# Kernel optimization log

Hardware: AMD Instinct MI355X
Metric: run time of the kernel (lower is better)

The kernel has to match this reference:

```python
import jax, jax.numpy as jnp
import numpy as np
from jax import lax

HID = 128      # GNN hidden dim (node_label_embedding_size)
EMB = 64       # char-CNN output (graph_node_label_representation_size)
N_LAYERS = 6
N_ETYPES = 12
CHAR_EMB = 16
KW = 5         # conv kernel width
LEAKY = 0.2


def _gru(x, h, k, rk, b):
    # keras-style GRU cell: gates z, r, candidate hh; new h = z*h + (1-z)*hh
    H = h.shape[-1]
    g = x @ k + b                       # [N, 3H]
    z = jax.nn.sigmoid(g[:, :H] + h @ rk[:, :H])
    r = jax.nn.sigmoid(g[:, H:2 * H] + h @ rk[:, H:2 * H])
    hh = jnp.tanh(g[:, 2 * H:] + (r * h) @ rk[:, 2 * H:])
    return z * h + (1.0 - z) * hh


def setup_inputs() -> dict:
    key = jax.random.key(0)
    ks = jax.random.split(key, 32)
    N, U, L, E, G = 100000, 20000, 16, 100000, 64
    inp = {}
    inp["graphs_in_batch"] = G
    inp["node_labels_unique"] = jax.random.randint(ks[0], (U, L), 0, 256, dtype=jnp.int32)
    inp["node_labels_index"] = jax.random.randint(ks[1], (N,), 0, U, dtype=jnp.int32)
    inp["node_to_graph"] = jnp.sort(jax.random.randint(ks[2], (N,), 0, G, dtype=jnp.int32))
    inp["regression_labels"] = jax.random.normal(ks[3], (G,), dtype=jnp.float32)
    for t in range(N_ETYPES):
        inp[f"adj_{t}"] = jax.random.randint(ks[4 + t], (E, 2), 0, N, dtype=jnp.int32)
    # learned params
    inp["char_embed"] = jax.random.normal(ks[16], (256, CHAR_EMB), dtype=jnp.float32) * 0.1
    inp["conv_w"] = jax.random.normal(ks[17], (KW, CHAR_EMB, EMB), dtype=jnp.float32) / np.sqrt(KW * CHAR_EMB)
    inp["conv_b"] = jnp.zeros((EMB,), dtype=jnp.float32)
    inp["W_msg"] = jax.random.normal(ks[18], (N_LAYERS, N_ETYPES, HID, HID), dtype=jnp.float32) / np.sqrt(HID)
    inp["gru_k"] = jax.random.normal(ks[19], (N_LAYERS, HID, 3 * HID), dtype=jnp.float32) / np.sqrt(HID)
    inp["gru_rk"] = jax.random.normal(ks[20], (N_LAYERS, HID, 3 * HID), dtype=jnp.float32) / np.sqrt(HID)
    inp["gru_b"] = jnp.zeros((N_LAYERS, 3 * HID), dtype=jnp.float32)
    inp["score_w"] = jax.random.normal(ks[21], (HID, 1), dtype=jnp.float32) / np.sqrt(HID)
    inp["score_b"] = jnp.zeros((1,), dtype=jnp.float32)
    inp["mlp_w1"] = jax.random.normal(ks[22], (HID, 128), dtype=jnp.float32) / np.sqrt(HID)
    inp["mlp_b1"] = jnp.zeros((128,), dtype=jnp.float32)
    inp["mlp_w2"] = jax.random.normal(ks[23], (128, 32), dtype=jnp.float32) / np.sqrt(128)
    inp["mlp_b2"] = jnp.zeros((32,), dtype=jnp.float32)
    inp["mlp_w3"] = jax.random.normal(ks[24], (32, 8), dtype=jnp.float32) / np.sqrt(32)
    inp["mlp_b3"] = jnp.zeros((8,), dtype=jnp.float32)
    inp["mlp_w4"] = jax.random.normal(ks[25], (8, 1), dtype=jnp.float32) / np.sqrt(8)
    inp["mlp_b4"] = jnp.zeros((1,), dtype=jnp.float32)
    return inp


def reference(graphs_in_batch, node_labels_unique, node_labels_index, node_to_graph,
              regression_labels, adj_0, adj_1, adj_2, adj_3, adj_4, adj_5, adj_6,
              adj_7, adj_8, adj_9, adj_10, adj_11, char_embed, conv_w, conv_b,
              W_msg, gru_k, gru_rk, gru_b, score_w, score_b,
              mlp_w1, mlp_b1, mlp_w2, mlp_b2, mlp_w3, mlp_b3, mlp_w4, mlp_b4):
    adj = jnp.stack([adj_0, adj_1, adj_2, adj_3, adj_4, adj_5, adj_6,
                     adj_7, adj_8, adj_9, adj_10, adj_11])  # [T, E, 2]
    # --- char-CNN node label embedding ---
    chars = char_embed[node_labels_unique]                  # [U, L, CE]
    conv = lax.conv_general_dilated(chars, conv_w, (1,), 'SAME',
                                    dimension_numbers=('NWC', 'WIO', 'NWC'))
    label_rep = jnp.max(jax.nn.relu(conv + conv_b), axis=1)  # [U, EMB]
    feats = label_rep[node_labels_index]                     # [N, EMB]
    N = feats.shape[0]
    # pad initial features up to hidden_dim
    h = jnp.pad(feats, ((0, 0), (0, HID - EMB)))             # [N, HID]
    src = adj[:, :, 0]                                       # [T, E]
    tgt = adj[:, :, 1].reshape(-1)                           # [T*E]
    # --- 6-layer GGNN message passing ---
    for layer in range(N_LAYERS):
        h_src = h[src]                                       # [T, E, HID]
        msgs = jnp.einsum('teh,thd->ted', h_src, W_msg[layer])
        agg = jax.ops.segment_sum(msgs.reshape(-1, HID), tgt, num_segments=N)
        h = _gru(agg, h, gru_k[layer], gru_rk[layer], gru_b[layer])
    # --- weighted-sum graph readout (sigmoid weights, leaky_relu MLP) ---
    scores = jax.nn.sigmoid(h @ score_w + score_b)           # [N, 1]
    v = jax.nn.leaky_relu(h @ mlp_w1 + mlp_b1, LEAKY)
    v = jax.nn.leaky_relu(v @ mlp_w2 + mlp_b2, LEAKY)
    v = jax.nn.leaky_relu(v @ mlp_w3 + mlp_b3, LEAKY)
    v = v @ mlp_w4 + mlp_b4                                  # [N, 1]
    graph_rep = jax.ops.segment_sum(scores * v, node_to_graph,
                                    num_segments=graphs_in_batch)  # [G, 1]
    return graph_rep
```

## Files before the change

kernel.cpp:

```cpp
#include <hip/hip_runtime.h>
#include <hip/hip_bf16.h>

#define LEAKY_SLOPE 0.2f

typedef short short8 __attribute__((ext_vector_type(8)));
typedef short short4v __attribute__((ext_vector_type(4)));
typedef float f32x4 __attribute__((ext_vector_type(4)));

static inline int cdiv(int a, int b) { return (a + b - 1) / b; }

__device__ __forceinline__ float bf2f(unsigned short s) {
    return __uint_as_float(((unsigned int)s) << 16);
}
__device__ __forceinline__ unsigned short f2bf(float x) {
    unsigned int u = __float_as_uint(x);
    return (unsigned short)((u + 0x7FFFu + ((u >> 16) & 1u)) >> 16);
}
__device__ __forceinline__ unsigned short bf_hi(float x, float& rem) {
    unsigned int u = __float_as_uint(x);
    unsigned int hi = (u + 0x7FFFu + ((u >> 16) & 1u)) & 0xFFFF0000u;
    rem = x - __uint_as_float(hi);
    return (unsigned short)(hi >> 16);
}

struct EdgeArgs {
    const int* adj[12];
    int E[12];
    int colOff[12];
};

__global__ __launch_bounds__(64) void label_kernel(
    const int* __restrict__ labels, const float* __restrict__ char_embed,
    const float* __restrict__ conv_w, const float* __restrict__ conv_b,
    float* __restrict__ lr, int U)
{
    __shared__ float ch[20][16];
    __shared__ int lab[16];
    const int u = blockIdx.x, t = threadIdx.x;
    {
        const int r = t >> 4, i = t & 15;
        const int padrow[4] = {0, 1, 18, 19};
        ch[padrow[r]][i] = 0.f;
    }
    if (t < 16) lab[t] = labels[(size_t)u * 16 + t];
    float cwr[5][16];
    #pragma unroll
    for (int k = 0; k < 5; ++k)
        #pragma unroll
        for (int i = 0; i < 16; ++i)
            cwr[k][i] = conv_w[(k * 16 + i) * 64 + t];
    __syncthreads();
    for (int j = t; j < 256; j += 64)
        ch[2 + (j >> 4)][j & 15] = char_embed[(size_t)lab[j >> 4] * 16 + (j & 15)];
    __syncthreads();
    float aw[16];
    const float b = conv_b[t];
    #pragma unroll
    for (int w = 0; w < 16; ++w) aw[w] = b;
    #pragma unroll
    for (int x = 0; x < 20; ++x)
        #pragma unroll
        for (int i = 0; i < 16; ++i) {
            const float chv = ch[x][i];
            #pragma unroll
            for (int k = 0; k < 5; ++k) {
                const int w = x - k;
                if (w >= 0 && w < 16) aw[w] += chv * cwr[k][i];
            }
        }
    float m = 0.f;
    #pragma unroll
    for (int w = 0; w < 16; ++w) m = fmaxf(m, aw[w]);
    lr[(size_t)u * 64 + t] = m;
}

__global__ void init_h_split(const int* __restrict__ idx, const float* __restrict__ lr,
                             unsigned short* __restrict__ hS, int N, int NP)
{
    const int i = blockIdx.x * blockDim.x + threadIdx.x;
    if (i >= NP * 16) return;
    const int n = i >> 4, kg = i & 15;
    const size_t u = (size_t)(n >> 7) * 32768 + (size_t)kg * 1024 + (size_t)(n & 127) * 8;
    short8 hi, lo;
    if (n < N && kg < 8) {
        const int id = idx[n];
        #pragma unroll
        for (int j = 0; j < 8; ++j) {
            const float v = lr[(size_t)id * 64 + kg * 8 + j];
            float r; hi[j] = (short)bf_hi(v, r); lo[j] = (short)f2bf(r);
        }
    } else {
        #pragma unroll
        for (int j = 0; j < 8; ++j) { hi[j] = 0; lo[j] = 0; }
    }
    *(short8*)(hS + u) = hi;
    *(short8*)(hS + u + 16384) = lo;
}

__global__ void hist_kernel(EdgeArgs ea, int* __restrict__ deg, int N)
{
    const int t = blockIdx.y;
    const int e = blockIdx.x * blockDim.x + threadIdx.x;
    if (e >= ea.E[t]) return;
    atomicAdd(&deg[(size_t)t * N + ea.adj[t][2 * e + 1]], 1);
}

__global__ __launch_bounds__(256) void scan_a(const int* __restrict__ deg,
                                              int* __restrict__ partial, int N, int nchunk)
{
    const int t = blockIdx.y, b = blockIdx.x;
    const int base = b * 2048;
    int s = 0;
    for (int i = threadIdx.x; i < 2048; i += 256) {
        const int g = base + i;
        if (g < N) s += deg[(size_t)t * N + g];
    }
    __shared__ int sm[256];
    sm[threadIdx.x] = s; __syncthreads();
    for (int off = 128; off > 0; off >>= 1) {
        if (threadIdx.x < off) sm[threadIdx.x] += sm[threadIdx.x + off];
        __syncthreads();
    }
    if (threadIdx.x == 0) partial[t * nchunk + b] = sm[0];
}

__global__ void scan_b(int* __restrict__ partial, int nchunk)
{
    const int t = threadIdx.x;
    if (t >= 12) return;
// ... 41 lines not shown
                            int* __restrict__ cursor, int* __restrict__ col, int N)
{
    const int t = blockIdx.y;
    const int e = blockIdx.x * blockDim.x + threadIdx.x;
    if (e >= ea.E[t]) return;
    const int s  = ea.adj[t][2 * e];
    const int tg = ea.adj[t][2 * e + 1];
    const int pos = rowptr[(size_t)t * (N + 1) + tg] + atomicAdd(&cursor[(size_t)t * N + tg], 1);
    col[ea.colOff[t] + pos] = s;
}

struct WSrc { const float* wmsg; const float* gk; const float* grk; const float* w1; };

__global__ void split_w_kernel(WSrc s, unsigned short* __restrict__ wb, int nmat)
{
    const int gidx = blockIdx.x * 256 + threadIdx.x;
    const int m = gidx >> 14, e = gidx & 16383;
    if (m >= nmat) return;
    const int kg = e >> 10, rem = e & 1023, c = rem >> 3, j = rem & 7;
    const int k = kg * 8 + j;
    float x;
    if (m < 72) x = s.wmsg[(size_t)m * 16384 + (size_t)k * 128 + c];
    else if (m < 108) {
        const int g = m - 72, layer = g / 6, r2 = g % 6;
        const float* base = (r2 < 3) ? s.gk : s.grk;
        const int slice = r2 % 3;
        x = base[(size_t)layer * 49152 + (size_t)k * 384 + slice * 128 + c];
    } else x = s.w1[(size_t)k * 128 + c];
    float r; const unsigned short hi = bf_hi(x, r);
    wb[(size_t)m * 32768 + e] = hi;
    wb[(size_t)m * 32768 + 16384 + e] = f2bf(r);
}

__device__ __forceinline__ void stage_panel(const unsigned short* __restrict__ g,
                                            unsigned short* __restrict__ lds, int tid)
{
    #pragma unroll
    for (int i = 0; i < 16; ++i) {
        const int uo = i * 2048 + tid * 8;
        *(short8*)(lds + uo) = *(const short8*)(g + uo);
    }
}

template<int NM>
__device__ __forceinline__ void mfma_pass(const unsigned short* __restrict__ lds,
                                          const unsigned short* const* Bs,
                                          f32x4 (&acc)[NM][4][4],
                                          int wr, int wc, int lrow, int lkg)
{
    #pragma unroll 1
    for (int c = 0; c < 4; ++c) {
        const int kg = c * 4 + lkg;
        short8 ah[4], al[4];
        #pragma unroll
        for (int m = 0; m < 4; ++m) {
            const int u = kg * 1024 + (wr * 64 + m * 16 + lrow) * 8;
            ah[m] = *(const short8*)(lds + u);
            al[m] = *(const short8*)(lds + u + 16384);
        }
        #pragma unroll
        for (int t = 0; t < NM; ++t) {
            const unsigned short* __restrict__ B = Bs[t];
            short8 bh[4], bl[4];
            #pragma unroll
            for (int n = 0; n < 4; ++n) {
                const int u = kg * 1024 + (wc * 64 + n * 16 + lrow) * 8;
                bh[n] = *(const short8*)(B + u);
                bl[n] = *(const short8*)(B + u + 16384);
            }
            #pragma unroll
            for (int m = 0; m < 4; ++m)
                #pragma unroll
                for (int n = 0; n < 4; ++n) {
                    acc[t][m][n] = __builtin_amdgcn_mfma_f32_16x16x32_bf16(ah[m], bh[n], acc[t][m][n], 0, 0, 0);
                    acc[t][m][n] = __builtin_amdgcn_mfma_f32_16x16x32_bf16(ah[m], bl[n], acc[t][m][n], 0, 0, 0);
                    acc[t][m][n] = __builtin_amdgcn_mfma_f32_16x16x32_bf16(al[m], bh[n], acc[t][m][n], 0, 0, 0);
                }
        }
    }
}

template<int NM>
__global__ __launch_bounds__(256) void msg_kernel(
    const unsigned short* __restrict__ hS,
    const unsigned short* __restrict__ B0, const unsigned short* __restrict__ B1,
    float* __restrict__ out0, float* __restrict__ out1)
{
    __shared__ unsigned short lds[32768];
    const int tid = threadIdx.x;
    stage_panel(hS + (size_t)blockIdx.x * 32768, lds, tid);
    const int wave = tid >> 6, lane = tid & 63;
    const int wr = wave >> 1, wc = wave & 1, lrow = lane & 15, lkg = lane >> 4;
    f32x4 acc[NM][4][4] = {};
    __syncthreads();
    const unsigned short* Bs[2] = {B0, B1};
    mfma_pass<NM>(lds, Bs, acc, wr, wc, lrow, lkg);
    const size_t rowBase = (size_t)blockIdx.x * 128;
    #pragma unroll
    for (int t = 0; t < NM; ++t) {
        float* __restrict__ op = t ? out1 : out0;
        #pragma unroll
        for (int m = 0; m < 4; ++m)
            #pragma unroll
            for (int n = 0; n < 4; ++n) {
                const int col = wc * 64 + n * 16 + lrow;
                #pragma unroll
                for (int i = 0; i < 4; ++i) {
                    const size_t r = rowBase + wr * 64 + m * 16 + lkg * 4 + i;
                    op[r * 128 + col] = acc[t][m][n][i];
                }
            }
    }
}

__global__ __launch_bounds__(256) void zr_kernel(
    const unsigned short* __restrict__ aT, const unsigned short* __restrict__ hS,
    const unsigned short* __restrict__ k0, const unsigned short* __restrict__ k1,
    const unsigned short* __restrict__ rk0, const unsigned short* __restrict__ rk1,
    const float* __restrict__ bias,
    float* __restrict__ zOut, unsigned short* __restrict__ rhS)
{
    __shared__ unsigned short lds[32768];
    const int tid = threadIdx.x;
    const size_t pbase = (size_t)blockIdx.x * 32768;
    const int wave = tid >> 6, lane = tid & 63;
    const int wr = wave >> 1, wc = wave & 1, lrow = lane & 15, lkg = lane >> 4;
    f32x4 acc[2][4][4] = {};

    stage_panel(aT + pbase, lds, tid);
    __syncthreads();
    { const unsigned short* Bs[2] = {k0, k1};  mfma_pass<2>(lds, Bs, acc, wr, wc, lrow, lkg); }
    __syncthreads();
    stage_panel(hS + pbase, lds, tid);
    __syncthreads();
    { const unsigned short* Bs[2] = {rk0, rk1}; mfma_pass<2>(lds, Bs, acc, wr, wc, lrow, lkg); }

    const size_t rowBase = (size_t)blockIdx.x * 128;
    #pragma unroll
    for (int m = 0; m < 4; ++m)
        #pragma unroll
        for (int n = 0; n < 4; ++n) {
            const int col = wc * 64 + n * 16 + lrow;
            #pragma unroll
            for (int i = 0; i < 4; ++i) {
                const int rl = wr * 64 + m * 16 + lkg * 4 + i;
                const float z = 1.f / (1.f + __expf(-(acc[0][m][n][i] + bias[col])));
                zOut[(rowBase + rl) * 128 + col] = z;
                const float v = 1.f / (1.f + __expf(-(acc[1][m][n][i] + bias[128 + col])));
                const int hu = (col >> 3) * 1024 + rl * 8 + (col & 7);
                const float hval = bf2f(lds[hu]) + bf2f(lds[hu + 16384]);
                const float rh = v * hval;
                float rem; const unsigned short hi = bf_hi(rh, rem);
                rhS[pbase + hu] = hi;
                rhS[pbase + hu + 16384] = f2bf(rem);
            }
        }
}

__global__ __launch_bounds__(256) void gemm_lds(
    const unsigned short* __restrict__ A1, const unsigned short* __restrict__ B1,
    const unsigned short* __restrict__ A2, const unsigned short* __restrict__ B2,
    const float* __restrict__ bias, float* __restrict__ outF, int act)
{
    __shared__ unsigned short lds[32768];
    const int tid = threadIdx.x;
    const size_t pbase = (size_t)blockIdx.x * 32768;
    const int wave = tid >> 6, lane = tid & 63;
    const int wr = wave >> 1, wc = wave & 1, lrow = lane & 15, lkg = lane >> 4;
    f32x4 acc[1][4][4] = {};

    stage_panel(A1 + pbase, lds, tid);
    __syncthreads();
    { const unsigned short* Bs[2] = {B1, nullptr}; mfma_pass<1>(lds, Bs, acc, wr, wc, lrow, lkg); }
    if (A2) {
        __syncthreads();
        stage_panel(A2 + pbase, lds, tid);
        __syncthreads();
        const unsigned short* Bs[2] = {B2, nullptr};
        mfma_pass<1>(lds, Bs, acc, wr, wc, lrow, lkg);
    }
    const size_t rowBase = (size_t)blockIdx.x * 128;
    #pragma unroll
    for (int m = 0; m < 4; ++m)
        #pragma unroll
        for (int n = 0; n < 4; ++n) {
            const int col = wc * 64 + n * 16 + lrow;
            #pragma unroll
            for (int i = 0; i < 4; ++i) {
                const int rl = wr * 64 + m * 16 + lkg * 4 + i;
                float v = acc[0][m][n][i];
                if (bias) v += bias[col];
                if (act == 1) v = v > 0.f ? v : LEAKY_SLOPE * v;
                outF[(rowBase + rl) * 128 + col] = v;
            }
        }
}

__global__ __launch_bounds__(256) void gather_csr(
    const int* __restrict__ rowptr, const int* __restrict__ col,
    const float* __restrict__ M, float* __restrict__ agg, int N, int accum)
{
    const int i = blockIdx.x * blockDim.x + threadIdx.x;
    const int n = i >> 5, q = i & 31;
    if (n >= N) return;
    float4 acc;
    if (accum) acc = *reinterpret_cast<const float4*>(agg + (size_t)n * 128 + (q << 2));
    else       acc = make_float4(0.f, 0.f, 0.f, 0.f);
    for (int s = rowptr[n]; s < rowptr[n + 1]; ++s) {
        const float4 v = *reinterpret_cast<const float4*>(M + (size_t)col[s] * 128 + (q << 2));
        acc.x += v.x; acc.y += v.y; acc.z += v.z; acc.w += v.w;
    }
    *reinterpret_cast<float4*>(agg + (size_t)n * 128 + (q << 2)) = acc;
}

__global__ __launch_bounds__(256) void gather2_csr(
    const int* __restrict__ rp0, const int* __restrict__ c0, const float* __restrict__ M0,
    const int* __restrict__ rp1, const int* __restrict__ c1, const float* __restrict__ M1,
    float* __restrict__ agg, int N, int accum)
{
    const int i = blockIdx.x * blockDim.x + threadIdx.x;
    const int n = i >> 5, q = i & 31;
    if (n >= N) return;
    float4 acc;
    if (accum) acc = *reinterpret_cast<const float4*>(agg + (size_t)n * 128 + (q << 2));
    else       acc = make_float4(0.f, 0.f, 0.f, 0.f);
    for (int s = rp0[n]; s < rp0[n + 1]; ++s) {
        const float4 v = *reinterpret_cast<const float4*>(M0 + (size_t)c0[s] * 128 + (q << 2));
        acc.x += v.x; acc.y += v.y; acc.z += v.z; acc.w += v.w;
    }
    for (int s = rp1[n]; s < rp1[n + 1]; ++s) {
        const float4 v = *reinterpret_cast<const float4*>(M1 + (size_t)c1[s] * 128 + (q << 2));
        acc.x += v.x; acc.y += v.y; acc.z += v.z; acc.w += v.w;
    }
    *reinterpret_cast<float4*>(agg + (size_t)n * 128 + (q << 2)) = acc;
}

__global__ __launch_bounds__(256) void gather_split_csr(
    const int* __restrict__ rp, const int* __restrict__ cl, const float* __restrict__ M,
    const float* __restrict__ agg, unsigned short* __restrict__ aT, int N, int NP)
{
    const int i = blockIdx.x * blockDim.x + threadIdx.x;
    const int n = i >> 5, q = i & 31;
    if (n >= NP) return;
    float4 a = make_float4(0.f, 0.f, 0.f, 0.f);
    if (n < N) {
        a = *reinterpret_cast<const float4*>(agg + (size_t)n * 128 + (q << 2));
        for (int s = rp[n]; s < rp[n + 1]; ++s) {
            const float4 v = *reinterpret_cast<const float4*>(M + (size_t)cl[s] * 128 + (q << 2));
            a.x += v.x; a.y += v.y; a.z += v.z; a.w += v.w;
        }
    }
    const size_t u = (size_t)(n >> 7) * 32768 + (size_t)(q >> 1) * 1024
                   + (size_t)(n & 127) * 8 + (q & 1) * 4;
    const float vv[4] = {a.x, a.y, a.z, a.w};
    short4v hi, lo;
    #pragma unroll
    for (int j = 0; j < 4; ++j) {
        float r; hi[j] = (short)bf_hi(vv[j], r); lo[j] = (short)f2bf(r);
    }
    *(short4v*)(aT + u) = hi;
    *(short4v*)(aT + u + 16384) = lo;
}

__global__ void gru_ew2_split(const float* __restrict__ Z, const float* __restrict__ G,
                              unsigned short* __restrict__ hS, int N)
{
    const int i = blockIdx.x * blockDim.x + threadIdx.x;
    if (i >= N * 16) return;
    const int n = i >> 4, kg = i & 15;
    const size_t u = (size_t)(n >> 7) * 32768 + (size_t)kg * 1024 + (size_t)(n & 127) * 8;
    const short8 hi = *(const short8*)(hS + u);
    const short8 lo = *(const short8*)(hS + u + 16384);
    const size_t ro = (size_t)n * 128 + kg * 8;
    short8 nhi, nlo;
    #pragma unroll
    for (int j = 0; j < 8; ++j) {
        const float h = bf2f((unsigned short)hi[j]) + bf2f((unsigned short)lo[j]);
        const float z = Z[ro + j];
        const float hn = z * h + (1.f - z) * tanhf(G[ro + j]);
        float r; nhi[j] = (short)bf_hi(hn, r); nlo[j] = (short)f2bf(r);
    }
    *(short8*)(hS + u) = nhi;
    *(short8*)(hS + u + 16384) = nlo;
}

__global__ __launch_bounds__(256) void final_kernel(
    const unsigned short* __restrict__ hS, const float* __restrict__ V1,
    const int* __restrict__ n2g,
    const float* __restrict__ w2, const float* __restrict__ b2,
    const float* __restrict__ w3, const float* __restrict__ b3,
    const float* __restrict__ w4, const float* __restrict__ b4,
    const float* __restrict__ score_w, const float* __restrict__ score_b,
    float* __restrict__ out, int N)
{
    const int n = blockIdx.x * blockDim.x + threadIdx.x;
    const int nc = n < N ? n : N - 1;
    const int g = n2g[nc];

    float sp = score_b[0];
    #pragma unroll 4
    for (int kg = 0; kg < 16; ++kg) {
        const size_t u = (size_t)(nc >> 7) * 32768 + (size_t)kg * 1024 + (size_t)(nc & 127) * 8;
        const short8 hh = *(const short8*)(hS + u);
        const short8 hl = *(const short8*)(hS + u + 16384);
        #pragma unroll
        for (int j = 0; j < 8; ++j)
            sp += (bf2f((unsigned short)hh[j]) + bf2f((unsigned short)hl[j])) * score_w[kg * 8 + j];
    }

    float V2[32];
    #pragma unroll
    for (int j = 0; j < 32; ++j) V2[j] = b2[j];
    #pragma unroll 2
    for (int k = 0; k < 128; k += 4) {
        const float4 v1 = *reinterpret_cast<const float4*>(V1 + (size_t)nc * 128 + k);
        const float vv[4] = {v1.x, v1.y, v1.z, v1.w};
        #pragma unroll
        for (int kk = 0; kk < 4; ++kk)
            #pragma unroll
            for (int j = 0; j < 32; ++j)
                V2[j] += vv[kk] * w2[(k + kk) * 32 + j];
    }
    #pragma unroll
    for (int j = 0; j < 32; ++j) { const float x = V2[j]; V2[j] = x > 0.f ? x : LEAKY_SLOPE * x; }

    float V3[8];
    #pragma unroll
    for (int j = 0; j < 8; ++j) V3[j] = b3[j];
    #pragma unroll
    for (int k = 0; k < 32; ++k)
        #pragma unroll
        for (int j = 0; j < 8; ++j) V3[j] += V2[k] * w3[k * 8 + j];
    #pragma unroll
    for (int j = 0; j < 8; ++j) { const float x = V3[j]; V3[j] = x > 0.f ? x : LEAKY_SLOPE * x; }

    float o4 = b4[0];
    #pragma unroll
// ... 30 lines not shown
        if (ea.E[t] > Emax) Emax = ea.E[t];
    }
    const float* char_embed = (const float*)d_in[17];
    const float* conv_w     = (const float*)d_in[18];
    const float* conv_b     = (const float*)d_in[19];
    const float* W_msg      = (const float*)d_in[20];
    const float* gru_k      = (const float*)d_in[21];
    const float* gru_rk     = (const float*)d_in[22];
    const float* gru_b      = (const float*)d_in[23];
    const float* score_w    = (const float*)d_in[24];
    const float* score_b    = (const float*)d_in[25];
    const float* w1 = (const float*)d_in[26];
    const float* b1 = (const float*)d_in[27];
    const float* w2 = (const float*)d_in[28];
    const float* b2 = (const float*)d_in[29];
    const float* w3 = (const float*)d_in[30];
    const float* b3 = (const float*)d_in[31];
    const float* w4 = (const float*)d_in[32];
    const float* b4 = (const float*)d_in[33];

    const int N = in_sizes[2];
    const int U = in_sizes[1] / 16;
    const int G = out_size;
    float* out = (float*)d_out;

    const int NPB = cdiv(N, 128);
    const int NP  = NPB * 128;
    const int NCHUNK = cdiv(N, 2048);
    const int NMAT = 109;

    float* ws = (float*)d_ws;
    size_t o = 0;
    float* lr   = ws + o; o += (size_t)U * 64;
    float* hSf  = ws + o; o += (size_t)NP * 128;
    float* Mf   = ws + o; o += (size_t)NP * 128;
    float* aggf = ws + o; o += (size_t)NP * 128;
    float* rhf  = ws + o; o += (size_t)NP * 128;
    float* wbf  = ws + o; o += (size_t)NMAT * 16384;
    int* rowptr = (int*)(ws + o);
    int* colarr = rowptr + (size_t)12 * (N + 1);
    const size_t total_bytes = o * sizeof(float)
        + ((size_t)12 * (N + 1) + (size_t)Etot) * sizeof(int);
    if (total_bytes > ws_size) return;

    unsigned short* hS  = (unsigned short*)hSf;
    unsigned short* aT  = (unsigned short*)Mf;
    unsigned short* rhS = (unsigned short*)rhf;
    unsigned short* wb  = (unsigned short*)wbf;

    int* deg     = (int*)Mf;
    int* cursor  = deg + (size_t)12 * N;
    int* partial = cursor + (size_t)12 * N;

    hipMemsetAsync(d_out, 0, (size_t)G * sizeof(float), stream);
    hipMemsetAsync(deg, 0, ((size_t)24 * N + 12 * NCHUNK) * sizeof(int), stream);

    {
        const dim3 ge(cdiv(Emax, 256), 12);
        const dim3 gs(NCHUNK, 12);
        hist_kernel<<<ge, 256, 0, stream>>>(ea, deg, N);
        scan_a<<<gs, 256, 0, stream>>>(deg, partial, N, NCHUNK);
        scan_b<<<1, 64, 0, stream>>>(partial, NCHUNK);
        scan_c<<<gs, 256, 0, stream>>>(deg, partial, rowptr, N, NCHUNK);
        fill_kernel<<<ge, 256, 0, stream>>>(ea, rowptr, cursor, colarr, N);
    }

    WSrc wsrc{W_msg, gru_k, gru_rk, w1};
    split_w_kernel<<<cdiv(NMAT * 16384, 256), 256, 0, stream>>>(wsrc, wb, NMAT);
    label_kernel<<<U, 64, 0, stream>>>(labels, char_embed, conv_w, conv_b, lr, U);
    init_h_split<<<cdiv(NP * 16, 256), 256, 0, stream>>>(nidx, lr, hS, N, NP);

    const int gatherBlocks = cdiv(N * 32, 256);
    const int gatherBlocksNP = cdiv(NP * 32, 256);
    const int ewBlocks = cdiv(N * 16, 256);
    auto rp  = [&](int t) { return rowptr + (size_t)t * (N + 1); };
    auto cp  = [&](int t) { return colarr + ea.colOff[t]; };
    auto wbm = [&](int m) { return wb + (size_t)m * 32768; };

    for (int layer = 0; layer < 6; ++layer) {
        const float* bl = gru_b + (size_t)layer * 384;
        const int mk = 72 + layer * 6;
        for (int p = 0; p < 5; ++p) {
            const int t0 = 2 * p, t1 = 2 * p + 1;
            msg_kernel<2><<<NPB, 256, 0, stream>>>(hS, wbm(layer * 12 + t0), wbm(layer * 12 + t1), Mf, rhf);
            gather2_csr<<<gatherBlocks, 256, 0, stream>>>(rp(t0), cp(t0), Mf,
                                                          rp(t1), cp(t1), rhf, aggf, N, p > 0);
        }
        msg_kernel<1><<<NPB, 256, 0, stream>>>(hS, wbm(layer * 12 + 10), nullptr, Mf, nullptr);
        gather_csr<<<gatherBlocks, 256, 0, stream>>>(rp(10), cp(10), Mf, aggf, N, 1);
        msg_kernel<1><<<NPB, 256, 0, stream>>>(hS, wbm(layer * 12 + 11), nullptr, rhf, nullptr);
        gather_split_csr<<<gatherBlocksNP, 256, 0, stream>>>(rp(11), cp(11), rhf, aggf, aT, N, NP);
        zr_kernel<<<NPB, 256, 0, stream>>>(aT, hS, wbm(mk + 0), wbm(mk + 1),
                                           wbm(mk + 3), wbm(mk + 4), bl, aggf, rhS);
        gemm_lds<<<NPB, 256, 0, stream>>>(aT, wbm(mk + 2), rhS, wbm(mk + 5), bl + 256, Mf, 0);
        gru_ew2_split<<<ewBlocks, 256, 0, stream>>>(aggf, Mf, hS, N);
    }
    gemm_lds<<<NPB, 256, 0, stream>>>(hS, wbm(108), nullptr, nullptr, b1, Mf, 1);
    final_kernel<<<cdiv(N, 256), 256, 0, stream>>>(hS, Mf, n2g, w2, b2, w3, b3, w4, b4,
                                                   score_w, score_b, out, N);
}
```

Baseline: 4.307 ms.

## Aggregate neighbor features before message GEMM and fuse GRU stages with pipelined LDS

Reorders message passing from transform-then-scatter to gather-then-transform: each block sums source node features per edge type via CSR, then runs one K=12*128 GEMM against the stacked per-type weights. This removes the per-type full-N message GEMMs and the fp32 message buffers that the gather kernels had to read back. Node state moves to a row-interleaved hi/lo bf16 layout, and the GRU is folded into two double-buffered GEMM kernels with swizzled LDS that also apply the elementwise update. The gather now runs inside the GEMM kernel with irregular per-row degree loops, so load imbalance and gather latency may stall the MFMA pipeline.

Result: slower. 4.518 ms (+4.9%).

```diff
diff --git a/kernel.cpp b/kernel.cpp
--- a/kernel.cpp
+++ b/kernel.cpp
@@ -4,7 +4,6 @@
 #define LEAKY_SLOPE 0.2f
 
 typedef short short8 __attribute__((ext_vector_type(8)));
-typedef short short4v __attribute__((ext_vector_type(4)));
 typedef float f32x4 __attribute__((ext_vector_type(4)));
 
 static inline int cdiv(int a, int b) { return (a + b - 1) / b; }
@@ -28,6 +27,7 @@
     int E[12];
     int colOff[12];
 };
+struct ColPtrs { const int* c[12]; };
 
 __global__ __launch_bounds__(64) void label_kernel(
     const int* __restrict__ labels, const float* __restrict__ char_embed,
@@ -74,14 +74,15 @@
     lr[(size_t)u * 64 + t] = m;
 }
 
-__global__ void init_h_split(const int* __restrict__ idx, const float* __restrict__ lr,
-                             unsigned short* __restrict__ hS, int N, int NP)
+__global__ void init_hP(const int* __restrict__ idx, const float* __restrict__ lr,
+                        unsigned short* __restrict__ hP, int N, int NP)
 {
     const int i = blockIdx.x * blockDim.x + threadIdx.x;
     if (i >= NP * 16) return;
     const int n = i >> 4, kg = i & 15;
-    const size_t u = (size_t)(n >> 7) * 32768 + (size_t)kg * 1024 + (size_t)(n & 127) * 8;
     short8 hi, lo;
+    #pragma unroll
+    for (int j = 0; j < 8; ++j) { hi[j] = 0; lo[j] = 0; }
     if (n < N && kg < 8) {
         const int id = idx[n];
         #pragma unroll
@@ -89,12 +90,9 @@
             const float v = lr[(size_t)id * 64 + kg * 8 + j];
             float r; hi[j] = (short)bf_hi(v, r); lo[j] = (short)f2bf(r);
         }
-    } else {
-        #pragma unroll
-        for (int j = 0; j < 8; ++j) { hi[j] = 0; lo[j] = 0; }
-    }
-    *(short8*)(hS + u) = hi;
-    *(short8*)(hS + u + 16384) = lo;
+    }
+    *(short8*)(hP + (size_t)n * 256 + kg * 16) = hi;
+    *(short8*)(hP + (size_t)n * 256 + kg * 16 + 8) = lo;
 }
 
 __global__ void hist_kernel(EdgeArgs ea, int* __restrict__ deg, int N)
@@ -202,110 +200,202 @@
     wb[(size_t)m * 32768 + 16384 + e] = f2bf(r);
 }
 
-__device__ __forceinline__ void stage_panel(const unsigned short* __restrict__ g,
-                                            unsigned short* __restrict__ lds, int tid)
-{
-    #pragma unroll
-    for (int i = 0; i < 16; ++i) {
-        const int uo = i * 2048 + tid * 8;
-        *(short8*)(lds + uo) = *(const short8*)(g + uo);
-    }
-}
-
-template<int NM>
-__device__ __forceinline__ void mfma_pass(const unsigned short* __restrict__ lds,
-                                          const unsigned short* const* Bs,
-                                          f32x4 (&acc)[NM][4][4],
-                                          int wr, int wc, int lrow, int lkg)
-{
-    #pragma unroll 1
-    for (int c = 0; c < 4; ++c) {
-        const int kg = c * 4 + lkg;
-        short8 ah[4], al[4];
-        #pragma unroll
-        for (int m = 0; m < 4; ++m) {
-            const int u = kg * 1024 + (wr * 64 + m * 16 + lrow) * 8;
-            ah[m] = *(const short8*)(lds + u);
-            al[m] = *(const short8*)(lds + u + 16384);
-        }
-        #pragma unroll
-        for (int t = 0; t < NM; ++t) {
-            const unsigned short* __restrict__ B = Bs[t];
-            short8 bh[4], bl[4];
-            #pragma unroll
-            for (int n = 0; n < 4; ++n) {
-                const int u = kg * 1024 + (wc * 64 + n * 16 + lrow) * 8;
-                bh[n] = *(const short8*)(B + u);
-                bl[n] = *(const short8*)(B + u + 16384);
-            }
-            #pragma unroll
-            for (int m = 0; m < 4; ++m)
-                #pragma unroll
-                for (int n = 0; n < 4; ++n) {
-                    acc[t][m][n] = __builtin_amdgcn_mfma_f32_16x16x32_bf16(ah[m], bh[n], acc[t][m][n], 0, 0, 0);
-                    acc[t][m][n] = __builtin_amdgcn_mfma_f32_16x16x32_bf16(ah[m], bl[n], acc[t][m][n], 0, 0, 0);
-                    acc[t][m][n] = __builtin_amdgcn_mfma_f32_16x16x32_bf16(al[m], bh[n], acc[t][m][n], 0, 0, 0);
-                }
-        }
-    }
-}
-
-template<int NM>
-__global__ __launch_bounds__(256) void msg_kernel(
-    const unsigned short* __restrict__ hS,
-    const unsigned short* __restrict__ B0, const unsigned short* __restrict__ B1,
-    float* __restrict__ out0, float* __restrict__ out1)
-{
-    __shared__ unsigned short lds[32768];
-    const int tid = threadIdx.x;
-    stage_panel(hS + (size_t)blockIdx.x * 32768, lds, tid);
+__global__ __launch_bounds__(256) void agg_kernel(
+    const unsigned short* __restrict__ hP,
+    const int* __restrict__ rowptr,
+    ColPtrs cps,
+    const unsigned short* __restrict__ wbL,
+    float* __restrict__ agg, int N)
+{
+    __shared__ unsigned short lds[2][8192];
+    const int tid = threadIdx.x, p = blockIdx.x;
+    const int r_loc = tid >> 1;
+    const int R = p * 128 + r_loc;
+    const int kp = (tid & 1) * 2;
     const int wave = tid >> 6, lane = tid & 63;
     const int wr = wave >> 1, wc = wave & 1, lrow = lane & 15, lkg = lane >> 4;
-    f32x4 acc[NM][4][4] = {};
+    f32x4 acc[4][4] = {};
+    float ga[2][8];
+
+    auto gather = [&](int s) {
+        const int t = s >> 2, q = s & 3;
+        #pragma unroll
+        for (int pc = 0; pc < 2; ++pc)
+            #pragma unroll
+            for (int j = 0; j < 8; ++j) ga[pc][j] = 0.f;
+        if (R < N) {
+            const int rbase = t * (N + 1) + R;
+            const int e1 = rowptr[rbase + 1];
+            const int* __restrict__ cl = cps.c[t];
+            for (int e = rowptr[rbase]; e < e1; ++e) {
+                const size_t sb = (size_t)cl[e] * 256 + (size_t)(q * 4 + kp) * 16;
+                #pragma unroll
+                for (int pc = 0; pc < 2; ++pc) {
+                    const short8 hh = *(const short8*)(hP + sb + pc * 16);
+                    const short8 hl = *(const short8*)(hP + sb + pc * 16 + 8);
+                    #pragma unroll
+                    for (int j = 0; j < 8; ++j)
+                        ga[pc][j] += bf2f((unsigned short)hh[j]) + bf2f((unsigned short)hl[j]);
+                }
+            }
+        }
+    };
+    auto stq = [&](int buf) {
+        unsigned short* L = lds[buf];
+        #pragma unroll
+        for (int pc = 0; pc < 2; ++pc) {
+            short8 hi, lo;
+            #pragma unroll
+            for (int j = 0; j < 8; ++j) {
+                float rem; hi[j] = (short)bf_hi(ga[pc][j], rem); lo[j] = (short)f2bf(rem);
+            }
+            const int kgl = kp + pc;
+            const int u = (kgl * 1024 + r_loc * 8) ^ (kgl << 3);
+            *(short8*)(L + u) = hi;
+            *(short8*)(L + u + 4096) = lo;
+        }
+    };
+    auto mfma_q = [&](int buf, int s) {
+        const unsigned short* L = lds[buf];
+        const unsigned short* __restrict__ B = wbL + (size_t)(s >> 2) * 32768;
+        const int q = s & 3;
+        short8 ah[4], al[4];
+        #pragma unroll
+        for (int m = 0; m < 4; ++m) {
+            const int u = ((lkg << 10) + (wr * 64 + m * 16 + lrow) * 8) ^ (lkg << 3);
+            ah[m] = *(const short8*)(L + u);
+            al[m] = *(const short8*)(L + u + 4096);
+        }
+        #pragma unroll
+        for (int n = 0; n < 4; ++n) {
+            const int ub = (q * 4 + lkg) * 1024 + (wc * 64 + n * 16 + lrow) * 8;
+            const short8 bh = *(const short8*)(B + ub);
+            const short8 bl = *(const short8*)(B + ub + 16384);
+            #pragma unroll
+            for (int m = 0; m < 4; ++m) {
+                acc[m][n] = __builtin_amdgcn_mfma_f32_16x16x32_bf16(ah[m], bh, acc[m][n], 0, 0, 0);
+                acc[m][n] = __builtin_amdgcn_mfma_f32_16x16x32_bf16(ah[m], bl, acc[m][n], 0, 0, 0);
+                acc[m][n] = __builtin_amdgcn_mfma_f32_16x16x32_bf16(al[m], bh, acc[m][n], 0, 0, 0);
+            }
+        }
+    };
+
+    gather(0); stq(0); gather(1);
     __syncthreads();
-    const unsigned short* Bs[2] = {B0, B1};
-    mfma_pass<NM>(lds, Bs, acc, wr, wc, lrow, lkg);
-    const size_t rowBase = (size_t)blockIdx.x * 128;
-    #pragma unroll
-    for (int t = 0; t < NM; ++t) {
-        float* __restrict__ op = t ? out1 : out0;
-        #pragma unroll
-        for (int m = 0; m < 4; ++m)
-            #pragma unroll
-            for (int n = 0; n < 4; ++n) {
-                const int col = wc * 64 + n * 16 + lrow;
-                #pragma unroll
-                for (int i = 0; i < 4; ++i) {
-                    const size_t r = rowBase + wr * 64 + m * 16 + lkg * 4 + i;
-                    op[r * 128 + col] = acc[t][m][n][i];
-                }
-            }
-    }
-}
-
-__global__ __launch_bounds__(256) void zr_kernel(
-    const unsigned short* __restrict__ aT, const unsigned short* __restrict__ hS,
+    #pragma unroll 1
+    for (int s = 0; s < 48; ++s) {
+        mfma_q(s & 1, s);
+        if (s < 47) {
+            stq((s + 1) & 1);
+            if (s < 46) gather(s + 2);
+            __syncthreads();
+        }
+    }
+
+    #pragma unroll
+    for (int m = 0; m < 4; ++m)
+        #pragma unroll
+        for (int n = 0; n < 4; ++n) {
+            const int col = wc * 64 + n * 16 + lrow;
+            #pragma unroll
+            for (int i = 0; i < 4; ++i) {
+                const size_t Rg = (size_t)p * 128 + wr * 64 + m * 16 + lkg * 4 + i;
+                agg[Rg * 128 + col] = acc[m][n][i];
+            }
+        }
+}
+
+__global__ __launch_bounds__(256) void zr2_kernel(
+    const float* __restrict__ aggf, const unsigned short* __restrict__ hP,
     const unsigned short* __restrict__ k0, const unsigned short* __restrict__ k1,
     const unsigned short* __restrict__ rk0, const unsigned short* __restrict__ rk1,
     const float* __restrict__ bias,
-    float* __restrict__ zOut, unsigned short* __restrict__ rhS)
-{
-    __shared__ unsigned short lds[32768];
-    const int tid = threadIdx.x;
-    const size_t pbase = (size_t)blockIdx.x * 32768;
+    float* __restrict__ Zf, unsigned short* __restrict__ rhP)
+{
+    __shared__ unsigned short lds[2][8192];
+    const int tid = threadIdx.x, p = blockIdx.x;
     const int wave = tid >> 6, lane = tid & 63;
     const int wr = wave >> 1, wc = wave & 1, lrow = lane & 15, lkg = lane >> 4;
     f32x4 acc[2][4][4] = {};
-
-    stage_panel(aT + pbase, lds, tid);
+    float fv[16];
+    short8 ph[2], pl[2];
+
+    auto ldq = [&](int s) {
+        const int q = s & 3;
+        #pragma unroll
+        for (int j = 0; j < 2; ++j) {
+            const int cid = j * 256 + tid, kgl = cid >> 7, row = cid & 127;
+            if (s < 4) {
+                const float* a = aggf + ((size_t)p * 128 + row) * 128 + q * 32 + kgl * 8;
+                const float4 v0 = *(const float4*)(a);
+                const float4 v1 = *(const float4*)(a + 4);
+                fv[j*8+0]=v0.x; fv[j*8+1]=v0.y; fv[j*8+2]=v0.z; fv[j*8+3]=v0.w;
+                fv[j*8+4]=v1.x; fv[j*8+5]=v1.y; fv[j*8+6]=v1.z; fv[j*8+7]=v1.w;
+            } else {
+                const unsigned short* hp = hP + ((size_t)p * 128 + row) * 256 + (q * 4 + kgl) * 16;
+                ph[j] = *(const short8*)(hp);
+                pl[j] = *(const short8*)(hp + 8);
+            }
+        }
+    };
+    auto stq = [&](int buf, int s) {
+        unsigned short* L = lds[buf];
+        #pragma unroll
+        for (int j = 0; j < 2; ++j) {
+            const int cid = j * 256 + tid, kgl = cid >> 7, row = cid & 127;
+            const int u = (kgl * 1024 + row * 8) ^ (kgl << 3);
+            short8 hi, lo;
+            if (s < 4) {
+                #pragma unroll
+                for (int q8 = 0; q8 < 8; ++q8) {
+                    float rem; hi[q8] = (short)bf_hi(fv[j*8+q8], rem); lo[q8] = (short)f2bf(rem);
+                }
+            } else { hi = ph[j]; lo = pl[j]; }
+            *(short8*)(L + u) = hi;
+            *(short8*)(L + u + 4096) = lo;
+        }
+    };
+    auto mfma_q = [&](int buf, int s) {
+        const unsigned short* L = lds[buf];
+        const int q = s & 3;
+        short8 ah[4], al[4];
+        #pragma unroll
+        for (int m = 0; m < 4; ++m) {
+            const int u = ((lkg << 10) + (wr * 64 + m * 16 + lrow) * 8) ^ (lkg << 3);
+            ah[m] = *(const short8*)(L + u);
+            al[m] = *(const short8*)(L + u + 4096);
+        }
+        const unsigned short* Bt[2] = { (s < 4) ? k0 : rk0, (s < 4) ? k1 : rk1 };
+        #pragma unroll
+        for (int t = 0; t < 2; ++t) {
+            const unsigned short* __restrict__ B = Bt[t];
+            #pragma unroll
+            for (int n = 0; n < 4; ++n) {
+                const int ub = (q * 4 + lkg) * 1024 + (wc * 64 + n * 16 + lrow) * 8;
+                const short8 bh = *(const short8*)(B + ub);
+                const short8 bl = *(const short8*)(B + ub + 16384);
+                #pragma unroll
+                for (int m = 0; m < 4; ++m) {
+                    acc[t][m][n] = __builtin_amdgcn_mfma_f32_16x16x32_bf16(ah[m], bh, acc[t][m][n], 0, 0, 0);
+                    acc[t][m][n] = __builtin_amdgcn_mfma_f32_16x16x32_bf16(ah[m], bl, acc[t][m][n], 0, 0, 0);
+                    acc[t][m][n] = __builtin_amdgcn_mfma_f32_16x16x32_bf16(al[m], bh, acc[t][m][n], 0, 0, 0);
+                }
+            }
+        }
+    };
+
+    ldq(0); stq(0, 0); ldq(1);
     __syncthreads();
-    { const unsigned short* Bs[2] = {k0, k1};  mfma_pass<2>(lds, Bs, acc, wr, wc, lrow, lkg); }
-    __syncthreads();
-    stage_panel(hS + pbase, lds, tid);
-    __syncthreads();
-    { const unsigned short* Bs[2] = {rk0, rk1}; mfma_pass<2>(lds, Bs, acc, wr, wc, lrow, lkg); }
-
-    const size_t rowBase = (size_t)blockIdx.x * 128;
+    #pragma unroll
+    for (int s = 0; s < 8; ++s) {
+        mfma_q(s & 1, s);
+        if (s < 7) {
+            stq((s + 1) & 1, s + 1);
+            if (s < 6) ldq(s + 2);
+            __syncthreads();
+        }
+    }
+
     #pragma unroll
     for (int m = 0; m < 4; ++m)
         #pragma unroll
@@ -314,42 +404,105 @@
             #pragma unroll
             for (int i = 0; i < 4; ++i) {
                 const int rl = wr * 64 + m * 16 + lkg * 4 + i;
+                const size_t R = (size_t)p * 128 + rl;
                 const float z = 1.f / (1.f + __expf(-(acc[0][m][n][i] + bias[col])));
-                zOut[(rowBase + rl) * 128 + col] = z;
-                const float v = 1.f / (1.f + __expf(-(acc[1][m][n][i] + bias[128 + col])));
-                const int hu = (col >> 3) * 1024 + rl * 8 + (col & 7);
-                const float hval = bf2f(lds[hu]) + bf2f(lds[hu + 16384]);
-                const float rh = v * hval;
-                float rem; const unsigned short hi = bf_hi(rh, rem);
-                rhS[pbase + hu] = hi;
-                rhS[pbase + hu + 16384] = f2bf(rem);
-            }
-        }
-}
-
-__global__ __launch_bounds__(256) void gemm_lds(
-    const unsigned short* __restrict__ A1, const unsigned short* __restrict__ B1,
-    const unsigned short* __restrict__ A2, const unsigned short* __restrict__ B2,
-    const float* __restrict__ bias, float* __restrict__ outF, int act)
-{
-    __shared__ unsigned short lds[32768];
-    const int tid = threadIdx.x;
-    const size_t pbase = (size_t)blockIdx.x * 32768;
+                Zf[R * 128 + col] = z;
+                const float r = 1.f / (1.f + __expf(-(acc[1][m][n][i] + bias[128 + col])));
+                const size_t hu = R * 256 + (size_t)(col >> 3) * 16 + (col & 7);
+                const float h = bf2f(hP[hu]) + bf2f(hP[hu + 8]);
+                float rem; const unsigned short hh = bf_hi(r * h, rem);
+                rhP[hu] = hh;
+                rhP[hu + 8] = f2bf(rem);
+            }
+        }
+}
+
+__global__ __launch_bounds__(256) void g2_kernel(
+    const float* __restrict__ aggf, const unsigned short* __restrict__ rhP,
+    const unsigned short* __restrict__ k2, const unsigned short* __restrict__ rk2,
+    const float* __restrict__ bias, const float* __restrict__ Zf,
+    unsigned short* __restrict__ hP)
+{
+    __shared__ unsigned short lds[2][8192];
+    const int tid = threadIdx.x, p = blockIdx.x;
     const int wave = tid >> 6, lane = tid & 63;
     const int wr = wave >> 1, wc = wave & 1, lrow = lane & 15, lkg = lane >> 4;
-    f32x4 acc[1][4][4] = {};
-
-    stage_panel(A1 + pbase, lds, tid);
+    f32x4 acc[4][4] = {};
+    float fv[16];
+    short8 ph[2], pl[2];
+
+    auto ldq = [&](int s) {
+        const int q = s & 3;
+        #pragma unroll
+        for (int j = 0; j < 2; ++j) {
+            const int cid = j * 256 + tid, kgl = cid >> 7, row = cid & 127;
+            if (s < 4) {
+                const float* a = aggf + ((size_t)p * 128 + row) * 128 + q * 32 + kgl * 8;
+                const float4 v0 = *(const float4*)(a);
+                const float4 v1 = *(const float4*)(a + 4);
+                fv[j*8+0]=v0.x; fv[j*8+1]=v0.y; fv[j*8+2]=v0.z; fv[j*8+3]=v0.w;
+                fv[j*8+4]=v1.x; fv[j*8+5]=v1.y; fv[j*8+6]=v1.z; fv[j*8+7]=v1.w;
+            } else {
+                const unsigned short* hp = rhP + ((size_t)p * 128 + row) * 256 + (q * 4 + kgl) * 16;
+                ph[j] = *(const short8*)(hp);
+                pl[j] = *(const short8*)(hp + 8);
+            }
+        }
+    };
+    auto stq = [&](int buf, int s) {
+        unsigned short* L = lds[buf];
+        #pragma unroll
+        for (int j = 0; j < 2; ++j) {
+            const int cid = j * 256 + tid, kgl = cid >> 7, row = cid & 127;
+            const int u = (kgl * 1024 + row * 8) ^ (kgl << 3);
+            short8 hi, lo;
+            if (s < 4) {
+                #pragma unroll
+                for (int q8 = 0; q8 < 8; ++q8) {
+                    float rem; hi[q8] = (short)bf_hi(fv[j*8+q8], rem); lo[q8] = (short)f2bf(rem);
+                }
+            } else { hi = ph[j]; lo = pl[j]; }
+            *(short8*)(L + u) = hi;
+            *(short8*)(L + u + 4096) = lo;
+        }
+    };
+    auto mfma_q = [&](int buf, int s) {
+        const unsigned short* L = lds[buf];
+        const int q = s & 3;
+        short8 ah[4], al[4];
+        #pragma unroll
+        for (int m = 0; m < 4; ++m) {
+            const int u = ((lkg << 10) + (wr * 64 + m * 16 + lrow) * 8) ^ (lkg << 3);
+            ah[m] = *(const short8*)(L + u);
+            al[m] = *(const short8*)(L + u + 4096);
+        }
+        const unsigned short* __restrict__ B = (s < 4) ? k2 : rk2;
+        #pragma unroll
+        for (int n = 0; n < 4; ++n) {
+            const int ub = (q * 4 + lkg) * 1024 + (wc * 64 + n * 16 + lrow) * 8;
+            const short8 bh = *(const short8*)(B + ub);
+            const short8 bl = *(const short8*)(B + ub + 16384);
+            #pragma unroll
+            for (int m = 0; m < 4; ++m) {
+                acc[m][n] = __builtin_amdgcn_mfma_f32_16x16x32_bf16(ah[m], bh, acc[m][n], 0, 0, 0);
+                acc[m][n] = __builtin_amdgcn_mfma_f32_16x16x32_bf16(ah[m], bl, acc[m][n], 0, 0, 0);
+                acc[m][n] = __builtin_amdgcn_mfma_f32_16x16x32_bf16(al[m], bh, acc[m][n], 0, 0, 0);
+            }
+        }
+    };
+
+    ldq(0); stq(0, 0); ldq(1);
     __syncthreads();
-    { const unsigned short* Bs[2] = {B1, nullptr}; mfma_pass<1>(lds, Bs, acc, wr, wc, lrow, lkg); }
-    if (A2) {
-        __syncthreads();
-        stage_panel(A2 + pbase, lds, tid);
-        __syncthreads();
-        const unsigned short* Bs[2] = {B2, nullptr};
-        mfma_pass<1>(lds, Bs, acc, wr, wc, lrow, lkg);
-    }
-    const size_t rowBase = (size_t)blockIdx.x * 128;
+    #pragma unroll
+    for (int s = 0; s < 8; ++s) {
+        mfma_q(s & 1, s);
+        if (s < 7) {
+            stq((s + 1) & 1, s + 1);
+            if (s < 6) ldq(s + 2);
+            __syncthreads();
+        }
+    }
+
     #pragma unroll
     for (int m = 0; m < 4; ++m)
         #pragma unroll
@@ -358,104 +511,101 @@
             #pragma unroll
             for (int i = 0; i < 4; ++i) {
                 const int rl = wr * 64 + m * 16 + lkg * 4 + i;
-                float v = acc[0][m][n][i];
-                if (bias) v += bias[col];
-                if (act == 1) v = v > 0.f ? v : LEAKY_SLOPE * v;
-                outF[(rowBase + rl) * 128 + col] = v;
-            }
-        }
-}
-
-__global__ __launch_bounds__(256) void gather_csr(
-    const int* __restrict__ rowptr, const int* __restrict__ col,
-    const float* __restrict__ M, float* __restrict__ agg, int N, int accum)
-{
-    const int i = blockIdx.x * blockDim.x + threadIdx.x;
-    const int n = i >> 5, q = i & 31;
-    if (n >= N) return;
-    float4 acc;
-    if (accum) acc = *reinterpret_cast<const float4*>(agg + (size_t)n * 128 + (q << 2));
-    else       acc = make_float4(0.f, 0.f, 0.f, 0.f);
-    for (int s = rowptr[n]; s < rowptr[n + 1]; ++s) {
-        const float4 v = *reinterpret_cast<const float4*>(M + (size_t)col[s] * 128 + (q << 2));
-        acc.x += v.x; acc.y += v.y; acc.z += v.z; acc.w += v.w;
-    }
-    *reinterpret_cast<float4*>(agg + (size_t)n * 128 + (q << 2)) = acc;
-}
-
-__global__ __launch_bounds__(256) void gather2_csr(
-    const int* __restrict__ rp0, const int* __restrict__ c0, const float* __restrict__ M0,
-    const int* __restrict__ rp1, const int* __restrict__ c1, const float* __restrict__ M1,
-    float* __restrict__ agg, int N, int accum)
-{
-    const int i = blockIdx.x * blockDim.x + threadIdx.x;
-    const int n = i >> 5, q = i & 31;
-    if (n >= N) return;
-    float4 acc;
-    if (accum) acc = *reinterpret_cast<const float4*>(agg + (size_t)n * 128 + (q << 2));
-    else       acc = make_float4(0.f, 0.f, 0.f, 0.f);
-    for (int s = rp0[n]; s < rp0[n + 1]; ++s) {
-        const float4 v = *reinterpret_cast<const float4*>(M0 + (size_t)c0[s] * 128 + (q << 2));
-        acc.x += v.x; acc.y += v.y; acc.z += v.z; acc.w += v.w;
-    }
-    for (int s = rp1[n]; s < rp1[n + 1]; ++s) {
-        const float4 v = *reinterpret_cast<const float4*>(M1 + (size_t)c1[s] * 128 + (q << 2));
-        acc.x += v.x; acc.y += v.y; acc.z += v.z; acc.w += v.w;
-    }
-    *reinterpret_cast<float4*>(agg + (size_t)n * 128 + (q << 2)) = acc;
-}
-
-__global__ __launch_bounds__(256) void gather_split_csr(
-    const int* __restrict__ rp, const int* __restrict__ cl, const float* __restrict__ M,
-    const float* __restrict__ agg, unsigned short* __restrict__ aT, int N, int NP)
-{
-    const int i = blockIdx.x * blockDim.x + threadIdx.x;
-    const int n = i >> 5, q = i & 31;
-    if (n >= NP) return;
-    float4 a = make_float4(0.f, 0.f, 0.f, 0.f);
-    if (n < N) {
-        a = *reinterpret_cast<const float4*>(agg + (size_t)n * 128 + (q << 2));
-        for (int s = rp[n]; s < rp[n + 1]; ++s) {
-            const float4 v = *reinterpret_cast<const float4*>(M + (size_t)cl[s] * 128 + (q << 2));
-            a.x += v.x; a.y += v.y; a.z += v.z; a.w += v.w;
-        }
-    }
-    const size_t u = (size_t)(n >> 7) * 32768 + (size_t)(q >> 1) * 1024
-                   + (size_t)(n & 127) * 8 + (q & 1) * 4;
-    const float vv[4] = {a.x, a.y, a.z, a.w};
-    short4v hi, lo;
-    #pragma unroll
-    for (int j = 0; j < 4; ++j) {
-        float r; hi[j] = (short)bf_hi(vv[j], r); lo[j] = (short)f2bf(r);
-    }
-    *(short4v*)(aT + u) = hi;
-    *(short4v*)(aT + u + 16384) = lo;
-}
-
-__global__ void gru_ew2_split(const float* __restrict__ Z, const float* __restrict__ G,
-                              unsigned short* __restrict__ hS, int N)
-{
-    const int i = blockIdx.x * blockDim.x + threadIdx.x;
-    if (i >= N * 16) return;
-    const int n = i >> 4, kg = i & 15;
-    const size_t u = (size_t)(n >> 7) * 32768 + (size_t)kg * 1024 + (size_t)(n & 127) * 8;
-    const short8 hi = *(const short8*)(hS + u);
-    const short8 lo = *(const short8*)(hS + u + 16384);
-    const size_t ro = (size_t)n * 128 + kg * 8;
-    short8 nhi, nlo;
-    #pragma unroll
-    for (int j = 0; j < 8; ++j) {
-        const float h = bf2f((unsigned short)hi[j]) + bf2f((unsigned short)lo[j]);
-        const float z = Z[ro + j];
-        const float hn = z * h + (1.f - z) * tanhf(G[ro + j]);
-        float r; nhi[j] = (short)bf_hi(hn, r); nlo[j] = (short)f2bf(r);
-    }
-    *(short8*)(hS + u) = nhi;
-    *(short8*)(hS + u + 16384) = nlo;
+                const size_t R = (size_t)p * 128 + rl;
+                const float g = acc[m][n][i] + bias[col];
+                const size_t hu = R * 256 + (size_t)(col >> 3) * 16 + (col & 7);
+                const float h = bf2f(hP[hu]) + bf2f(hP[hu + 8]);
+                const float z = Zf[R * 128 + col];
+                const float hn = z * h + (1.f - z) * tanhf(g);
+                float rem; const unsigned short hh = bf_hi(hn, rem);
+                hP[hu] = hh;
+                hP[hu + 8] = f2bf(rem);
+            }
+        }
+}
+
+__global__ __launch_bounds__(256) void v1_kernel(
+    const unsigned short* __restrict__ hP, const unsigned short* __restrict__ w1b,
+    const float* __restrict__ bias, float* __restrict__ outF)
+{
+    __shared__ unsigned short lds[2][8192];
+    const int tid = threadIdx.x, p = blockIdx.x;
+    const int wave = tid >> 6, lane = tid & 63;
+    const int wr = wave >> 1, wc = wave & 1, lrow = lane & 15, lkg = lane >> 4;
+    f32x4 acc[4][4] = {};
+    short8 ph[2], pl[2];
+
+    auto ldq = [&](int s) {
+        #pragma unroll
+        for (int j = 0; j < 2; ++j) {
+            const int cid = j * 256 + tid, kgl = cid >> 7, row = cid & 127;
+            const unsigned short* hp = hP + ((size_t)p * 128 + row) * 256 + (s * 4 + kgl) * 16;
+            ph[j] = *(const short8*)(hp);
+            pl[j] = *(const short8*)(hp + 8);
+        }
+    };
+    auto stq = [&](int buf) {
+        unsigned short* L = lds[buf];
+        #pragma unroll
+        for (int j = 0; j < 2; ++j) {
+            const int cid = j * 256 + tid, kgl = cid >> 7, row = cid & 127;
+            const int u = (kgl * 1024 + row * 8) ^ (kgl << 3);
+            *(short8*)(L + u) = ph[j];
+            *(short8*)(L + u + 4096) = pl[j];
+        }
+    };
+    auto mfma_q = [&](int buf, int s) {
+        const unsigned short* L = lds[buf];
+        short8 ah[4], al[4];
+        #pragma unroll
+        for (int m = 0; m < 4; ++m) {
+            const int u = ((lkg << 10) + (wr * 64 + m * 16 + lrow) * 8) ^ (lkg << 3);
+            ah[m] = *(const short8*)(L + u);
+            al[m] = *(const short8*)(L + u + 4096);
+        }
+        #pragma unroll
+        for (int n = 0; n < 4; ++n) {
+            const int ub = (s * 4 + lkg) * 1024 + (wc * 64 + n * 16 + lrow) * 8;
+            const short8 bh = *(const short8*)(w1b + ub);
+            const short8 bl = *(const short8*)(w1b + ub + 16384);
+            #pragma unroll
+            for (int m = 0; m < 4; ++m) {
+                acc[m][n] = __builtin_amdgcn_mfma_f32_16x16x32_bf16(ah[m], bh, acc[m][n], 0, 0, 0);
+                acc[m][n] = __builtin_amdgcn_mfma_f32_16x16x32_bf16(ah[m], bl, acc[m][n], 0, 0, 0);
+                acc[m][n] = __builtin_amdgcn_mfma_f32_16x16x32_bf16(al[m], bh, acc[m][n], 0, 0, 0);
+            }
+        }
+    };
+
+    ldq(0); stq(0); ldq(1);
+    __syncthreads();
+    #pragma unroll
+    for (int s = 0; s < 4; ++s) {
+        mfma_q(s & 1, s);
+        if (s < 3) {
+            stq((s + 1) & 1);
+            if (s < 2) ldq(s + 2);
+            __syncthreads();
+        }
+    }
+
+    #pragma unroll
+    for (int m = 0; m < 4; ++m)
+        #pragma unroll
+        for (int n = 0; n < 4; ++n) {
+            const int col = wc * 64 + n * 16 + lrow;
+            #pragma unroll
+            for (int i = 0; i < 4; ++i) {
+                const size_t R = (size_t)p * 128 + wr * 64 + m * 16 + lkg * 4 + i;
+                float v = acc[m][n][i] + bias[col];
+                v = v > 0.f ? v : LEAKY_SLOPE * v;
+                outF[R * 128 + col] = v;
+            }
+        }
 }
 
 __global__ __launch_bounds__(256) void final_kernel(
-    const unsigned short* __restrict__ hS, const float* __restrict__ V1,
+    const unsigned short* __restrict__ hP, const float* __restrict__ V1,
     const int* __restrict__ n2g,
     const float* __restrict__ w2, const float* __restrict__ b2,
     const float* __restrict__ w3, const float* __restrict__ b3,
@@ -470,9 +620,9 @@
     float sp = score_b[0];
     #pragma unroll 4
     for (int kg = 0; kg < 16; ++kg) {
-        const size_t u = (size_t)(nc >> 7) * 32768 + (size_t)kg * 1024 + (size_t)(nc & 127) * 8;
-        const short8 hh = *(const short8*)(hS + u);
-        const short8 hl = *(const short8*)(hS + u + 16384);
+        const size_t hu = (size_t)nc * 256 + kg * 16;
+        const short8 hh = *(const short8*)(hP + hu);
+        const short8 hl = *(const short8*)(hP + hu + 8);
         #pragma unroll
         for (int j = 0; j < 8; ++j)
             sp += (bf2f((unsigned short)hh[j]) + bf2f((unsigned short)hl[j])) * score_w[kg * 8 + j];
@@ -569,10 +719,10 @@
     float* ws = (float*)d_ws;
     size_t o = 0;
     float* lr   = ws + o; o += (size_t)U * 64;
-    float* hSf  = ws + o; o += (size_t)NP * 128;
-    float* Mf   = ws + o; o += (size_t)NP * 128;
+    float* hPf  = ws + o; o += (size_t)NP * 128;
     float* aggf = ws + o; o += (size_t)NP * 128;
-    float* rhf  = ws + o; o += (size_t)NP * 128;
+    float* Zf   = ws + o; o += (size_t)NP * 128;
+    float* rhPf = ws + o; o += (size_t)NP * 128;
     float* wbf  = ws + o; o += (size_t)NMAT * 16384;
     int* rowptr = (int*)(ws + o);
     int* colarr = rowptr + (size_t)12 * (N + 1);
@@ -580,12 +730,11 @@
         + ((size_t)12 * (N + 1) + (size_t)Etot) * sizeof(int);
     if (total_bytes > ws_size) return;
 
-    unsigned short* hS  = (unsigned short*)hSf;
-    unsigned short* aT  = (unsigned short*)Mf;
-    unsigned short* rhS = (unsigned short*)rhf;
+    unsigned short* hP  = (unsigned short*)hPf;
+    unsigned short* rhP = (unsigned short*)rhPf;
     unsigned short* wb  = (unsigned short*)wbf;
 
-    int* deg     = (int*)Mf;
+    int* deg     = (int*)Zf;
     int* cursor  = deg + (size_t)12 * N;
     int* partial = cursor + (size_t)12 * N;
 
@@ -605,34 +754,23 @@
     WSrc wsrc{W_msg, gru_k, gru_rk, w1};
     split_w_kernel<<<cdiv(NMAT * 16384, 256), 256, 0, stream>>>(wsrc, wb, NMAT);
     label_kernel<<<U, 64, 0, stream>>>(labels, char_embed, conv_w, conv_b, lr, U);
-    init_h_split<<<cdiv(NP * 16, 256), 256, 0, stream>>>(nidx, lr, hS, N, NP);
-
-    const int gatherBlocks = cdiv(N * 32, 256);
-    const int gatherBlocksNP = cdiv(NP * 32, 256);
-    const int ewBlocks = cdiv(N * 16, 256);
-    auto rp  = [&](int t) { return rowptr + (size_t)t * (N + 1); };
-    auto cp  = [&](int t) { return colarr + ea.colOff[t]; };
+    init_hP<<<cdiv(NP * 16, 256), 256, 0, stream>>>(nidx, lr, hP, N, NP);
+
+    ColPtrs cps;
+    for (int t = 0; t < 12; ++t) cps.c[t] = colarr + ea.colOff[t];
     auto wbm = [&](int m) { return wb + (size_t)m * 32768; };
 
     for (int layer = 0; layer < 6; ++layer) {
         const float* bl = gru_b + (size_t)layer * 384;
         const int mk = 72 + layer * 6;
-        for (int p = 0; p < 5; ++p) {
-            const int t0 = 2 * p, t1 = 2 * p + 1;
-            msg_kernel<2><<<NPB, 256, 0, stream>>>(hS, wbm(layer * 12 + t0), wbm(layer * 12 + t1), Mf, rhf);
-            gather2_csr<<<gatherBlocks, 256, 0, stream>>>(rp(t0), cp(t0), Mf,
-                                                          rp(t1), cp(t1), rhf, aggf, N, p > 0);
-        }
-        msg_kernel<1><<<NPB, 256, 0, stream>>>(hS, wbm(layer * 12 + 10), nullptr, Mf, nullptr);
-        gather_csr<<<gatherBlocks, 256, 0, stream>>>(rp(10), cp(10), Mf, aggf, N, 1);
-        msg_kernel<1><<<NPB, 256, 0, stream>>>(hS, wbm(layer * 12 + 11), nullptr, rhf, nullptr);
-        gather_split_csr<<<gatherBlocksNP, 256, 0, stream>>>(rp(11), cp(11), rhf, aggf, aT, N, NP);
-        zr_kernel<<<NPB, 256, 0, stream>>>(aT, hS, wbm(mk + 0), wbm(mk + 1),
-                                           wbm(mk + 3), wbm(mk + 4), bl, aggf, rhS);
-        gemm_lds<<<NPB, 256, 0, stream>>>(aT, wbm(mk + 2), rhS, wbm(mk + 5), bl + 256, Mf, 0);
-        gru_ew2_split<<<ewBlocks, 256, 0, stream>>>(aggf, Mf, hS, N);
-    }
-    gemm_lds<<<NPB, 256, 0, stream>>>(hS, wbm(108), nullptr, nullptr, b1, Mf, 1);
-    final_kernel<<<cdiv(N, 256), 256, 0, stream>>>(hS, Mf, n2g, w2, b2, w3, b3, w4, b4,
+        agg_kernel<<<NPB, 256, 0, stream>>>(hP, rowptr, cps,
+                                            wbm(layer * 12), aggf, N);
+        zr2_kernel<<<NPB, 256, 0, stream>>>(aggf, hP, wbm(mk + 0), wbm(mk + 1),
+                                            wbm(mk + 3), wbm(mk + 4), bl, Zf, rhP);
+        g2_kernel<<<NPB, 256, 0, stream>>>(aggf, rhP, wbm(mk + 2), wbm(mk + 5),
+                                           bl + 256, Zf, hP);
+    }
+    v1_kernel<<<NPB, 256, 0, stream>>>(hP, wbm(108), b1, Zf);
+    final_kernel<<<cdiv(N, 256), 256, 0, stream>>>(hP, Zf, n2g, w2, b2, w3, b3, w4, b4,
                                                    score_w, score_b, out, N);
 }
```
